# Kernel tuning notes

Measured on AMD Instinct MI355X. Metric: run time of the kernel, lower is better.

The kernel has to match this reference:

```python
import jax, jax.numpy as jnp
import numpy as np

# Static config (matches init_kwargs)
B = 1; Z = 64; H = 64; W = 64; C = 96
NH = 3; WS = 4; SS = 2
N = WS ** 3                      # tokens per 3D window = 64
NW = (Z // WS) * (H // WS) * (W // WS)   # num windows = 4096
SCALE = (C // NH) ** -0.5
EPS = 1e-5


def _rel_pos_index():
    # same construction as WindowAttention3D.__init__ (torch.meshgrid default 'ij')
    coords = np.stack(np.meshgrid(np.arange(WS), np.arange(WS), np.arange(WS), indexing='ij'))
    cf = coords.reshape(3, -1)                       # (3, N)
    rc = (cf[:, :, None] - cf[:, None, :]).transpose(1, 2, 0)  # (N, N, 3)
    rc[:, :, 0] += WS - 1; rc[:, :, 1] += WS - 1; rc[:, :, 2] += WS - 1
    rc[:, :, 0] *= (2 * WS - 1) ** 2
    rc[:, :, 1] *= (2 * WS - 1)
    return rc.sum(-1)                                # (N, N) int


def _attn_mask():
    # shifted-window mask, as in SwinTransformerBlock3D.__init__
    img = np.zeros((Z, H, W), dtype=np.float32)
    sl = (slice(0, -WS), slice(-WS, -SS), slice(-SS, None))
    cnt = 0
    for z in sl:
        for h in sl:
            for w in sl:
                img[z, h, w] = cnt
                cnt += 1
    mw = img.reshape(Z // WS, WS, H // WS, WS, W // WS, WS)
    mw = mw.transpose(0, 2, 4, 1, 3, 5).reshape(-1, N)        # (nW, N)
    am = mw[:, None, :] - mw[:, :, None]                      # (nW, N, N)
    return np.where(am != 0, np.float32(-100.0), np.float32(0.0))


REL_IDX = jnp.asarray(_rel_pos_index())        # (N, N) int32, closed-over constant
ATTN_MASK = jnp.asarray(_attn_mask())          # (nW, N, N) float32


def _layernorm(x, g, b):
    m = x.mean(-1, keepdims=True)
    v = ((x - m) ** 2).mean(-1, keepdims=True)
    return (x - m) * jax.lax.rsqrt(v + EPS) * g + b


def _window_partition(x):
    # (B, Z, H, W, C) -> (B*nW, N, C)
    x = x.reshape(B, Z // WS, WS, H // WS, WS, W // WS, WS, C)
    return x.transpose(0, 1, 3, 5, 2, 4, 6, 7).reshape(-1, N, C)


def _window_reverse(wins):
    # (B*nW, N, C) -> (B, Z, H, W, C)
    x = wins.reshape(B, Z // WS, H // WS, W // WS, WS, WS, WS, C)
    return x.transpose(0, 1, 4, 2, 5, 3, 6, 7).reshape(B, Z, H, W, C)


def setup_inputs() -> dict:
    key = jax.random.key(0)
    ks = jax.random.split(key, 8)
    d = {
        'x': jax.random.normal(ks[0], (B, Z * H * W, C), jnp.float32),
        'norm1_w': jnp.ones((C,), jnp.float32),
        'norm1_b': jnp.zeros((C,), jnp.float32),
        'qkv_w': jax.random.normal(ks[1], (3 * C, C), jnp.float32) * 0.02,
        'qkv_b': jnp.zeros((3 * C,), jnp.float32),
        'rel_bias': jax.random.normal(ks[2], ((2 * WS - 1) ** 3, NH), jnp.float32) * 0.02,
        'proj_w': jax.random.normal(ks[3], (C, C), jnp.float32) * 0.02,
        'proj_b': jnp.zeros((C,), jnp.float32),
        'norm2_w': jnp.ones((C,), jnp.float32),
        'norm2_b': jnp.zeros((C,), jnp.float32),
        'fc1_w': jax.random.normal(ks[4], (4 * C, C), jnp.float32) * 0.02,
        'fc1_b': jnp.zeros((4 * C,), jnp.float32),
        'fc2_w': jax.random.normal(ks[5], (C, 4 * C), jnp.float32) * 0.02,
        'fc2_b': jnp.zeros((C,), jnp.float32),
    }
    return d


def reference(x, norm1_w, norm1_b, qkv_w, qkv_b, rel_bias, proj_w, proj_b,
              norm2_w, norm2_b, fc1_w, fc1_b, fc2_w, fc2_b):
    shortcut = x
    h = _layernorm(x, norm1_w, norm1_b).reshape(B, Z, H, W, C)
    # cyclic shift (SW-MSA)
    h = jnp.roll(h, (-SS, -SS, -SS), axis=(1, 2, 3))
    xw = _window_partition(h)                                  # (B*nW, N, C)
    qkv = (xw @ qkv_w.T + qkv_b).reshape(-1, N, 3, NH, C // NH)
    qkv = qkv.transpose(2, 0, 3, 1, 4)                         # (3, B_, NH, N, hd)
    q, k, v = qkv[0] * SCALE, qkv[1], qkv[2]
    attn = jnp.einsum('bhnd,bhmd->bhnm', q, k)                 # (B_, NH, N, N)
    bias = rel_bias[REL_IDX.reshape(-1)].reshape(N, N, NH).transpose(2, 0, 1)
    attn = attn + bias[None]
    attn = attn.reshape(B, NW, NH, N, N) + ATTN_MASK[None, :, None]
    attn = jax.nn.softmax(attn.reshape(-1, NH, N, N), axis=-1)
    out = jnp.einsum('bhnm,bhmd->bhnd', attn, v)
    out = out.transpose(0, 2, 1, 3).reshape(-1, N, C)
    out = out @ proj_w.T + proj_b
    h = _window_reverse(out)
    h = jnp.roll(h, (SS, SS, SS), axis=(1, 2, 3)).reshape(B, Z * H * W, C)
    x = shortcut + h                                            # residual (drop_path=0)
    y = _layernorm(x, norm2_w, norm2_b)
    y = jax.nn.gelu(y @ fc1_w.T + fc1_b, approximate=False)
    y = y @ fc2_w.T + fc2_b
    return x + y
```

## Files before the change

kernel.cpp:

```cpp
#include <hip/hip_runtime.h>

typedef __attribute__((ext_vector_type(8))) short short8;
typedef __attribute__((ext_vector_type(4))) float f32x4;
typedef __attribute__((ext_vector_type(4))) unsigned short ush4;

static __device__ __forceinline__ unsigned short f2bf(float f) {
  return (unsigned short)((__builtin_bit_cast(unsigned int, f) + 0x8000u) >> 16);
}
static __device__ __forceinline__ unsigned cvtpk(float a, float b) {
  unsigned r;
  asm("v_cvt_pk_bf16_f32 %0, %1, %2" : "=v"(r) : "v"(a), "v"(b));
  return r;
}

constexpr float LOG2E = 1.4426950408889634f;
constexpr float QSCL = 0.17677669529663687f * LOG2E;
constexpr int XP = 104;
constexpr int KP = 104;
constexpr int VTP = 72;

static __device__ __forceinline__ int frag_src(int o, int K) {
  const int j = o & 7;
  const int lane = (o >> 3) & 63;
  const int f = o >> 9;
  const int nks = K >> 5;
  const int ks = f % nks;
  const int t = f / nks;
  const int row = t * 16 + (lane & 15);
  const int k = ks * 32 + (lane >> 4) * 8 + j;
  return row * K + k;
}

__global__ void prep_kernel(const float* __restrict__ qkvw, const float* __restrict__ projw,
                            const float* __restrict__ fc1w, const float* __restrict__ fc2w,
                            const float* __restrict__ relbias,
                            unsigned short* __restrict__ ws, float* __restrict__ tab) {
  int i = blockIdx.x * 256 + threadIdx.x;
  if (i < 27648) ws[i] = f2bf(qkvw[frag_src(i, 96)]);
  if (i < 9216)  ws[27648 + i] = f2bf(projw[frag_src(i, 96)]);
  if (i < 36864) {
    ws[36864 + i] = f2bf(fc1w[frag_src(i, 96)]);
    ws[73728 + i] = f2bf(fc2w[frag_src(i, 384)]);
  }
  if (i < 98304) {
    const int r = i & 3, kgi = (i >> 2) & 3, q = (i >> 4) & 63, nt = (i >> 10) & 3;
    const int vh = i >> 12;
    const int h = vh % 3, v = vh / 3;
    const int key = nt * 16 + kgi * 4 + r;
    const bool bz = v & 4, bh = v & 2, bw = v & 1;
    const int iz = q >> 4, ih = (q >> 2) & 3, iw = q & 3;
    const int jz = key >> 4, jh = (key >> 2) & 3, jw = key & 3;
    const int idx = (iz - jz + 3) * 49 + (ih - jh + 3) * 7 + (iw - jw + 3);
    const int ci = (bz ? (iz < 2 ? 9 : 18) : 0) + (bh ? (ih < 2 ? 3 : 6) : 0) +
                   (bw ? (iw < 2 ? 1 : 2) : 0);
    const int cj = (bz ? (jz < 2 ? 9 : 18) : 0) + (bh ? (jh < 2 ? 3 : 6) : 0) +
                   (bw ? (jw < 2 ? 1 : 2) : 0);
    tab[i] = (relbias[idx * 3 + h] + (ci != cj ? -100.f : 0.f)) * LOG2E;
  }
}

__global__ __launch_bounds__(256, 3) void fused_kernel(
    const float* __restrict__ x,
    const float* __restrict__ n1w, const float* __restrict__ n1b,
    const float* __restrict__ qkvb, const float* __restrict__ tab,
    const float* __restrict__ projb,
    const float* __restrict__ n2w, const float* __restrict__ n2b,
    const float* __restrict__ b1, const float* __restrict__ b2,
    const unsigned short* __restrict__ wq, const unsigned short* __restrict__ wp,
    const unsigned short* __restrict__ w1, const unsigned short* __restrict__ w2,
    float* __restrict__ out) {
  __shared__ unsigned short Xo[64 * XP];
  __shared__ unsigned short Kb[64 * KP];
  __shared__ unsigned short Vt[96 * VTP];

  const int tid = threadIdx.x;
  const int bid = blockIdx.x;
  const int wz = bid >> 8, wh = (bid >> 4) & 15, ww = bid & 15;
  const int wave = tid >> 6, lane = tid & 63;
  const int ln = lane & 15, kg = lane >> 4;

  {
    const int n = tid >> 2, part = tid & 3;
    const int lz = n >> 4, lh = (n >> 2) & 3, lw = n & 3;
    const int sz = (wz * 4 + lz + 2) & 63;
    const int sh = (wh * 4 + lh + 2) & 63;
    const int sw = (ww * 4 + lw + 2) & 63;
    const float* px = x + (size_t)((sz * 64 + sh) * 64 + sw) * 96 + part * 24;
    float4 v[6];
#pragma unroll
    for (int j = 0; j < 6; ++j) v[j] = ((const float4*)px)[j];
    float s = 0.f, sq = 0.f;
#pragma unroll
    for (int j = 0; j < 6; ++j) {
      s += v[j].x + v[j].y + v[j].z + v[j].w;
      sq += v[j].x * v[j].x + v[j].y * v[j].y + v[j].z * v[j].z + v[j].w * v[j].w;
    }
    s += __shfl_xor(s, 1);  s += __shfl_xor(s, 2);
    sq += __shfl_xor(sq, 1); sq += __shfl_xor(sq, 2);
    const float mean = s * (1.f / 96.f);
    const float var = sq * (1.f / 96.f) - mean * mean;
    const float rs = rsqrtf(var + 1e-5f);
    const float4* g4 = (const float4*)(n1w + part * 24);
    const float4* b4 = (const float4*)(n1b + part * 24);
#pragma unroll
    for (int j = 0; j < 6; ++j) {
      float4 g = g4[j], b = b4[j];
      uint2 o;
      o.x = cvtpk((v[j].x - mean) * rs * g.x + b.x, (v[j].y - mean) * rs * g.y + b.y);
      o.y = cvtpk((v[j].z - mean) * rs * g.z + b.z, (v[j].w - mean) * rs * g.w + b.w);
      *(uint2*)&Xo[n * XP + part * 24 + j * 4] = o;
    }
  }

  short8 qa[3];
  {
    short8 a[3];
#pragma unroll
    for (int ks = 0; ks < 3; ++ks)
      a[ks] = *(const short8*)&Xo[(wave * 16 + ln) * XP + ks * 32 + kg * 8];
#pragma unroll
    for (int half = 0; half < 2; ++half) {
      short8 wf[9];
#pragma unroll
      for (int f = 0; f < 9; ++f)
        wf[f] = *(const short8*)&wq[(size_t)(half * 9 + f) * 512 + lane * 8];
#pragma unroll
      for (int t = 0; t < 3; ++t) {
        const int nt = half * 3 + t;
        const int oc = nt * 16 + ln;
        f32x4 acc = {0.f, 0.f, 0.f, 0.f};
#pragma unroll
        for (int ks = 0; ks < 3; ++ks)
          acc = __builtin_amdgcn_mfma_f32_16x16x32_bf16(a[ks], wf[t * 3 + ks], acc, 0, 0, 0);
        const float bias = qkvb[oc];
#pragma unroll
        for (int r = 0; r < 4; ++r)
          Kb[(wave * 16 + kg * 4 + r) * KP + oc] = f2bf((acc[r] + bias) * QSCL);
      }
    }
#pragma unroll
    for (int h = 0; h < 3; ++h)
      qa[h] = *(const short8*)&Kb[(wave * 16 + ln) * KP + h * 32 + kg * 8];
#pragma unroll
    for (int half = 0; half < 2; ++half) {
      short8 wf[9];
#pragma unroll
      for (int f = 0; f < 9; ++f)
        wf[f] = *(const short8*)&wq[(size_t)(18 + half * 9 + f) * 512 + lane * 8];
#pragma unroll
      for (int t = 0; t < 3; ++t) {
        const int nt = half * 3 + t;
        const int oc = 96 + nt * 16 + ln;
        f32x4 acc = {0.f, 0.f, 0.f, 0.f};
#pragma unroll
        for (int ks = 0; ks < 3; ++ks)
          acc = __builtin_amdgcn_mfma_f32_16x16x32_bf16(a[ks], wf[t * 3 + ks], acc, 0, 0, 0);
        const float bias = qkvb[oc];
#pragma unroll
        for (int r = 0; r < 4; ++r)
          Kb[(wave * 16 + kg * 4 + r) * KP + nt * 16 + ln] = f2bf(acc[r] + bias);
      }
    }
#pragma unroll
    for (int half = 0; half < 2; ++half) {
      short8 wf[9];
#pragma unroll
      for (int f = 0; f < 9; ++f)
        wf[f] = *(const short8*)&wq[(size_t)(36 + half * 9 + f) * 512 + lane * 8];
#pragma unroll
      for (int t = 0; t < 3; ++t) {
        const int nt = half * 3 + t;
        const int oc = 192 + nt * 16 + ln;
        f32x4 acc = {0.f, 0.f, 0.f, 0.f};
#pragma unroll
        for (int ks = 0; ks < 3; ++ks)
          acc = __builtin_amdgcn_mfma_f32_16x16x32_bf16(a[ks], wf[t * 3 + ks], acc, 0, 0, 0);
        const float bias = qkvb[oc];
        uint2 u;
        u.x = cvtpk(acc[0] + bias, acc[1] + bias);
        u.y = cvtpk(acc[2] + bias, acc[3] + bias);
        *(uint2*)&Vt[(nt * 16 + ln) * VTP + wave * 16 + kg * 4] = u;
      }
    }
  }
  __syncthreads();

  const int vv = ((wz == 15) ? 4 : 0) | ((wh == 15) ? 2 : 0) | ((ww == 15) ? 1 : 0);
  const float* tb0 = tab + (size_t)(vv * 3) * 4096;
  const int rowbase = wave * 16 + kg * 4;
  const int lA = ((kg & 1) << 5) + ln;
  const int lB = lA + 16;
#pragma unroll
  for (int h = 0; h < 3; ++h) {
    const float* tb = tb0 + h * 4096;
    f32x4 trow[4];
#pragma unroll
    for (int nt = 0; nt < 4; ++nt)
      trow[nt] = *(const f32x4*)(tb + nt * 1024 + (wave * 16 + ln) * 16 + kg * 4);
    short8 kf[4];
#pragma unroll
    for (int nt = 0; nt < 4; ++nt)
      kf[nt] = *(const short8*)&Kb[(nt * 16 + ln) * KP + h * 32 + kg * 8];
    f32x4 e[4];
#pragma unroll
    for (int nt = 0; nt < 4; ++nt) {
      f32x4 z = {0.f, 0.f, 0.f, 0.f};
      f32x4 st = __builtin_amdgcn_mfma_f32_16x16x32_bf16(kf[nt], qa[h], z, 0, 0, 0);
#pragma unroll
      for (int r = 0; r < 4; ++r)
        e[nt][r] = __builtin_amdgcn_exp2f(st[r] + trow[nt][r]);
    }
    float hs = 0.f;
#pragma unroll
    for (int nt = 0; nt < 4; ++nt)
#pragma unroll
      for (int r = 0; r < 4; ++r) hs += e[nt][r];
    hs += __shfl_xor(hs, 16);
    hs += __shfl_xor(hs, 32);
    const float inv = __builtin_amdgcn_rcpf(hs);
    unsigned pp[4][2];
#pragma unroll
    for (int nt = 0; nt < 4; ++nt) {
      pp[nt][0] = cvtpk(e[nt][0] * inv, e[nt][1] * inv);
      pp[nt][1] = cvtpk(e[nt][2] * inv, e[nt][3] * inv);
    }
    short8 paf[2];
#pragma unroll
    for (int ks = 0; ks < 2; ++ks) {
      const unsigned a0 = __shfl((int)pp[2 * ks][0], lA);
      const unsigned a1 = __shfl((int)pp[2 * ks][1], lA);
      const unsigned a2 = __shfl((int)pp[2 * ks][0], lB);
      const unsigned a3 = __shfl((int)pp[2 * ks][1], lB);
      const unsigned b0 = __shfl((int)pp[2 * ks + 1][0], lA);
      const unsigned b1 = __shfl((int)pp[2 * ks + 1][1], lA);
      const unsigned b2 = __shfl((int)pp[2 * ks + 1][0], lB);
      const unsigned b3 = __shfl((int)pp[2 * ks + 1][1], lB);
      const bool hi = (kg >> 1) != 0;
      uint4 wv;
      wv.x = hi ? b0 : a0;
      wv.y = hi ? b1 : a1;
      wv.z = hi ? b2 : a2;
      wv.w = hi ? b3 : a3;
      paf[ks] = __builtin_bit_cast(short8, wv);
    }
#pragma unroll
    for (int dt = 0; dt < 2; ++dt) {
      f32x4 oacc = {0.f, 0.f, 0.f, 0.f};
#pragma unroll
      for (int ks = 0; ks < 2; ++ks) {
        short8 vb = *(const short8*)&Vt[(h * 32 + dt * 16 + ln) * VTP + ks * 32 + kg * 8];
        oacc = __builtin_amdgcn_mfma_f32_16x16x32_bf16(paf[ks], vb, oacc, 0, 0, 0);
      }
#pragma unroll
      for (int r = 0; r < 4; ++r)
        Xo[(rowbase + r) * XP + h * 32 + dt * 16 + ln] = f2bf(oacc[r]);
    }
  }

  float vout[6][4];
  int gtok[4];
  float mean_[4], rs_[4];
  {
#pragma unroll
    for (int r = 0; r < 4; ++r) {
      const int n = rowbase + r;
      const int lz = n >> 4, lh = (n >> 2) & 3, lw = n & 3;
      const int oz = (wz * 4 + lz + 2) & 63;
      const int oh = (wh * 4 + lh + 2) & 63;
      const int ow = (ww * 4 + lw + 2) & 63;
      gtok[r] = (oz * 64 + oh) * 64 + ow;
    }
    float xr[6][4];
#pragma unroll
    for (int nt = 0; nt < 6; ++nt)
#pragma unroll
      for (int r = 0; r < 4; ++r)
        xr[nt][r] = x[(size_t)gtok[r] * 96 + nt * 16 + ln];
    short8 oa[3];
#pragma unroll
    for (int ks = 0; ks < 3; ++ks)
      oa[ks] = *(const short8*)&Xo[(wave * 16 + ln) * XP + ks * 32 + kg * 8];
#pragma unroll
    for (int half = 0; half < 2; ++half) {
      short8 wf[9];
#pragma unroll
      for (int f = 0; f < 9; ++f)
        wf[f] = *(const short8*)&wp[(size_t)(half * 9 + f) * 512 + lane * 8];
#pragma unroll
      for (int t = 0; t < 3; ++t) {
        const int nt = half * 3 + t;
        const int col = nt * 16 + ln;
        f32x4 acc = {0.f, 0.f, 0.f, 0.f};
#pragma unroll
        for (int ks = 0; ks < 3; ++ks)
          acc = __builtin_amdgcn_mfma_f32_16x16x32_bf16(oa[ks], wf[t * 3 + ks], acc, 0, 0, 0);
        const float pbv = projb[col];
#pragma unroll
        for (int r = 0; r < 4; ++r)
          vout[nt][r] = xr[nt][r] + acc[r] + pbv;
      }
    }
#pragma unroll
    for (int r = 0; r < 4; ++r) {
      float s = 0.f, sq = 0.f;
#pragma unroll
      for (int nt = 0; nt < 6; ++nt) { s += vout[nt][r]; sq += vout[nt][r] * vout[nt][r]; }
      s += __shfl_xor(s, 1);  s += __shfl_xor(s, 2);
      s += __shfl_xor(s, 4);  s += __shfl_xor(s, 8);
      sq += __shfl_xor(sq, 1); sq += __shfl_xor(sq, 2);
      sq += __shfl_xor(sq, 4); sq += __shfl_xor(sq, 8);
      const float mean = s * (1.f / 96.f);
      const float var = sq * (1.f / 96.f) - mean * mean;
      mean_[r] = mean;
      rs_[r] = rsqrtf(var + 1e-5f);
    }
#pragma unroll
    for (int nt = 0; nt < 6; ++nt) {
      const int col = nt * 16 + ln;
      const float gw = n2w[col], gb = n2b[col];
#pragma unroll
      for (int r = 0; r < 4; ++r) {
        const float xl = (vout[nt][r] - mean_[r]) * rs_[r] * gw + gb;
        Xo[(rowbase + r) * XP + col] = f2bf(xl);
      }
    }
  }

  short8 a2[3];
#pragma unroll
  for (int ks = 0; ks < 3; ++ks)
    a2[ks] = *(const short8*)&Xo[(wave * 16 + ln) * XP + ks * 32 + kg * 8];

  __syncthreads();

  f32x4 facc[6];
#pragma unroll
  for (int nt = 0; nt < 6; ++nt) facc[nt] = (f32x4){0.f, 0.f, 0.f, 0.f};
#pragma unroll 1
  for (int c = 0; c < 4; ++c) {
#pragma unroll
    for (int half = 0; half < 2; ++half) {
      short8 wf1[9];
#pragma unroll
      for (int f = 0; f < 9; ++f)
        wf1[f] = *(const short8*)&w1[(size_t)(c * 18 + half * 9 + f) * 512 + lane * 8];
#pragma unroll
      for (int t = 0; t < 3; ++t) {
        const int nt2 = half * 3 + t;
        f32x4 acc = {0.f, 0.f, 0.f, 0.f};
#pragma unroll
        for (int ks = 0; ks < 3; ++ks)
          acc = __builtin_amdgcn_mfma_f32_16x16x32_bf16(a2[ks], wf1[t * 3 + ks], acc, 0, 0, 0);
        const float bb = b1[c * 96 + nt2 * 16 + ln];
#pragma unroll
        for (int r = 0; r < 4; ++r) {
          const float v = acc[r] + bb;
          const float t2 = v * v;
          float p = fmaf(0.004287f, t2, -0.05694f);
          p = fmaf(p, t2, 0.3952f);
          float phi = fmaf(p, v, 0.5f);
          phi = fminf(fmaxf(phi, 0.f), 1.f);
          Kb[(rowbase + r) * KP + nt2 * 16 + ln] = f2bf(v * phi);
        }
      }
    }
#pragma unroll
    for (int ks2 = 0; ks2 < 3; ++ks2) {
      short8 wf2[6];
#pragma unroll
      for (int nt = 0; nt < 6; ++nt)
        wf2[nt] = *(const short8*)&w2[(size_t)(nt * 12 + c * 3 + ks2) * 512 + lane * 8];
      short8 pa = *(const short8*)&Kb[(wave * 16 + ln) * KP + ks2 * 32 + kg * 8];
#pragma unroll
      for (int nt = 0; nt < 6; ++nt)
        facc[nt] = __builtin_amdgcn_mfma_f32_16x16x32_bf16(pa, wf2[nt], facc[nt], 0, 0, 0);
    }
  }
#pragma unroll
  for (int nt = 0; nt < 6; ++nt) {
    const int col = nt * 16 + ln;
    const float bb = b2[col];
#pragma unroll
    for (int r = 0; r < 4; ++r)
      out[(size_t)gtok[r] * 96 + col] = vout[nt][r] + facc[nt][r] + bb;
  }
}

extern "C" void kernel_launch(void* const* d_in, const int* in_sizes, int n_in,
                              void* d_out, int out_size, void* d_ws, size_t ws_size,
                              hipStream_t stream) {
  const float* x    = (const float*)d_in[0];
  const float* n1w  = (const float*)d_in[1];
  const float* n1b  = (const float*)d_in[2];
  const float* qkvw = (const float*)d_in[3];
  const float* qkvb = (const float*)d_in[4];
  const float* relb = (const float*)d_in[5];
  const float* pw   = (const float*)d_in[6];
  const float* pb   = (const float*)d_in[7];
  const float* n2w  = (const float*)d_in[8];
  const float* n2b  = (const float*)d_in[9];
  const float* w1   = (const float*)d_in[10];
  const float* b1   = (const float*)d_in[11];
  const float* w2   = (const float*)d_in[12];
  const float* b2   = (const float*)d_in[13];
  float* out = (float*)d_out;

  unsigned short* wsq = (unsigned short*)d_ws;
  unsigned short* wsp = wsq + 27648;
  unsigned short* ws1 = wsp + 9216;
  unsigned short* ws2 = ws1 + 36864;
  float* tab = (float*)(wsq + 110592);

  hipLaunchKernelGGL(prep_kernel, dim3(384), dim3(256), 0, stream,
                     qkvw, pw, w1, w2, relb, wsq, tab);
  hipLaunchKernelGGL(fused_kernel, dim3(4096), dim3(256), 0, stream,
                     x, n1w, n1b, qkvb, tab, pb, n2w, n2b, b1, b2,
                     wsq, wsp, ws1, ws2, out);
}
```

Baseline: 157.7 us.

## Cut register pressure to raise occupancy to four blocks per CU

Raises the launch bound from 3 to 4 blocks per CU. To fit that budget it shrinks the live register set. Weight fragments are now loaded in smaller groups, and the attention K and table loads move inside the per-tile loop. The post-attention residual is no longer held in a 24-float array: it is written to the output buffer, reread for LayerNorm2, and read back again for the final residual add. This trades extra global memory traffic and smaller load batches, which hide latency less well, for more resident waves.

```diff
diff --git a/kernel.cpp b/kernel.cpp
--- a/kernel.cpp
+++ b/kernel.cpp
@@ -2,7 +2,6 @@
 
 typedef __attribute__((ext_vector_type(8))) short short8;
 typedef __attribute__((ext_vector_type(4))) float f32x4;
-typedef __attribute__((ext_vector_type(4))) unsigned short ush4;
 
 static __device__ __forceinline__ unsigned short f2bf(float f) {
   return (unsigned short)((__builtin_bit_cast(unsigned int, f) + 0x8000u) >> 16);
@@ -59,7 +58,7 @@
   }
 }
 
-__global__ __launch_bounds__(256, 3) void fused_kernel(
+__global__ __launch_bounds__(256, 4) void fused_kernel(
     const float* __restrict__ x,
     const float* __restrict__ n1w, const float* __restrict__ n1b,
     const float* __restrict__ qkvb, const float* __restrict__ tab,
@@ -119,14 +118,14 @@
     for (int ks = 0; ks < 3; ++ks)
       a[ks] = *(const short8*)&Xo[(wave * 16 + ln) * XP + ks * 32 + kg * 8];
 #pragma unroll
-    for (int half = 0; half < 2; ++half) {
-      short8 wf[9];
-#pragma unroll
-      for (int f = 0; f < 9; ++f)
-        wf[f] = *(const short8*)&wq[(size_t)(half * 9 + f) * 512 + lane * 8];
-#pragma unroll
-      for (int t = 0; t < 3; ++t) {
-        const int nt = half * 3 + t;
+    for (int g = 0; g < 3; ++g) {
+      short8 wf[6];
+#pragma unroll
+      for (int f = 0; f < 6; ++f)
+        wf[f] = *(const short8*)&wq[(size_t)(g * 6 + f) * 512 + lane * 8];
+#pragma unroll
+      for (int t = 0; t < 2; ++t) {
+        const int nt = g * 2 + t;
         const int oc = nt * 16 + ln;
         f32x4 acc = {0.f, 0.f, 0.f, 0.f};
 #pragma unroll
@@ -142,14 +141,14 @@
     for (int h = 0; h < 3; ++h)
       qa[h] = *(const short8*)&Kb[(wave * 16 + ln) * KP + h * 32 + kg * 8];
 #pragma unroll
-    for (int half = 0; half < 2; ++half) {
-      short8 wf[9];
-#pragma unroll
-      for (int f = 0; f < 9; ++f)
-        wf[f] = *(const short8*)&wq[(size_t)(18 + half * 9 + f) * 512 + lane * 8];
-#pragma unroll
-      for (int t = 0; t < 3; ++t) {
-        const int nt = half * 3 + t;
+    for (int g = 0; g < 3; ++g) {
+      short8 wf[6];
+#pragma unroll
+      for (int f = 0; f < 6; ++f)
+        wf[f] = *(const short8*)&wq[(size_t)(18 + g * 6 + f) * 512 + lane * 8];
+#pragma unroll
+      for (int t = 0; t < 2; ++t) {
+        const int nt = g * 2 + t;
         const int oc = 96 + nt * 16 + ln;
         f32x4 acc = {0.f, 0.f, 0.f, 0.f};
 #pragma unroll
@@ -162,14 +161,14 @@
       }
     }
 #pragma unroll
-    for (int half = 0; half < 2; ++half) {
-      short8 wf[9];
-#pragma unroll
-      for (int f = 0; f < 9; ++f)
-        wf[f] = *(const short8*)&wq[(size_t)(36 + half * 9 + f) * 512 + lane * 8];
-#pragma unroll
-      for (int t = 0; t < 3; ++t) {
-        const int nt = half * 3 + t;
+    for (int g = 0; g < 3; ++g) {
+      short8 wf[6];
+#pragma unroll
+      for (int f = 0; f < 6; ++f)
+        wf[f] = *(const short8*)&wq[(size_t)(36 + g * 6 + f) * 512 + lane * 8];
+#pragma unroll
+      for (int t = 0; t < 2; ++t) {
+        const int nt = g * 2 + t;
         const int oc = 192 + nt * 16 + ln;
         f32x4 acc = {0.f, 0.f, 0.f, 0.f};
 #pragma unroll
@@ -193,22 +192,16 @@
 #pragma unroll
   for (int h = 0; h < 3; ++h) {
     const float* tb = tb0 + h * 4096;
-    f32x4 trow[4];
-#pragma unroll
-    for (int nt = 0; nt < 4; ++nt)
-      trow[nt] = *(const f32x4*)(tb + nt * 1024 + (wave * 16 + ln) * 16 + kg * 4);
-    short8 kf[4];
-#pragma unroll
-    for (int nt = 0; nt < 4; ++nt)
-      kf[nt] = *(const short8*)&Kb[(nt * 16 + ln) * KP + h * 32 + kg * 8];
     f32x4 e[4];
 #pragma unroll
     for (int nt = 0; nt < 4; ++nt) {
+      short8 kf = *(const short8*)&Kb[(nt * 16 + ln) * KP + h * 32 + kg * 8];
+      f32x4 trow = *(const f32x4*)(tb + nt * 1024 + (wave * 16 + ln) * 16 + kg * 4);
       f32x4 z = {0.f, 0.f, 0.f, 0.f};
-      f32x4 st = __builtin_amdgcn_mfma_f32_16x16x32_bf16(kf[nt], qa[h], z, 0, 0, 0);
+      f32x4 st = __builtin_amdgcn_mfma_f32_16x16x32_bf16(kf, qa[h], z, 0, 0, 0);
 #pragma unroll
       for (int r = 0; r < 4; ++r)
-        e[nt][r] = __builtin_amdgcn_exp2f(st[r] + trow[nt][r]);
+        e[nt][r] = __builtin_amdgcn_exp2f(st[r] + trow[r]);
     }
     float hs = 0.f;
 #pragma unroll
@@ -257,7 +250,6 @@
     }
   }
 
-  float vout[6][4];
   int gtok[4];
   float mean_[4], rs_[4];
   {
@@ -270,25 +262,20 @@
       const int ow = (ww * 4 + lw + 2) & 63;
       gtok[r] = (oz * 64 + oh) * 64 + ow;
     }
-    float xr[6][4];
-#pragma unroll
-    for (int nt = 0; nt < 6; ++nt)
-#pragma unroll
-      for (int r = 0; r < 4; ++r)
-        xr[nt][r] = x[(size_t)gtok[r] * 96 + nt * 16 + ln];
     short8 oa[3];
 #pragma unroll
     for (int ks = 0; ks < 3; ++ks)
       oa[ks] = *(const short8*)&Xo[(wave * 16 + ln) * XP + ks * 32 + kg * 8];
-#pragma unroll
-    for (int half = 0; half < 2; ++half) {
-      short8 wf[9];
-#pragma unroll
-      for (int f = 0; f < 9; ++f)
-        wf[f] = *(const short8*)&wp[(size_t)(half * 9 + f) * 512 + lane * 8];
-#pragma unroll
-      for (int t = 0; t < 3; ++t) {
-        const int nt = half * 3 + t;
+    float s_[4] = {0.f, 0.f, 0.f, 0.f}, sq_[4] = {0.f, 0.f, 0.f, 0.f};
+#pragma unroll
+    for (int g = 0; g < 3; ++g) {
+      short8 wf[6];
+#pragma unroll
+      for (int f = 0; f < 6; ++f)
+        wf[f] = *(const short8*)&wp[(size_t)(g * 6 + f) * 512 + lane * 8];
+#pragma unroll
+      for (int t = 0; t < 2; ++t) {
+        const int nt = g * 2 + t;
         const int col = nt * 16 + ln;
         f32x4 acc = {0.f, 0.f, 0.f, 0.f};
 #pragma unroll
@@ -296,15 +283,17 @@
           acc = __builtin_amdgcn_mfma_f32_16x16x32_bf16(oa[ks], wf[t * 3 + ks], acc, 0, 0, 0);
         const float pbv = projb[col];
 #pragma unroll
-        for (int r = 0; r < 4; ++r)
-          vout[nt][r] = xr[nt][r] + acc[r] + pbv;
+        for (int r = 0; r < 4; ++r) {
+          const float v = x[(size_t)gtok[r] * 96 + col] + acc[r] + pbv;
+          s_[r] += v;
+          sq_[r] += v * v;
+          out[(size_t)gtok[r] * 96 + col] = v;
+        }
       }
     }
 #pragma unroll
     for (int r = 0; r < 4; ++r) {
-      float s = 0.f, sq = 0.f;
-#pragma unroll
-      for (int nt = 0; nt < 6; ++nt) { s += vout[nt][r]; sq += vout[nt][r] * vout[nt][r]; }
+      float s = s_[r], sq = sq_[r];
       s += __shfl_xor(s, 1);  s += __shfl_xor(s, 2);
       s += __shfl_xor(s, 4);  s += __shfl_xor(s, 8);
       sq += __shfl_xor(sq, 1); sq += __shfl_xor(sq, 2);
@@ -314,15 +303,16 @@
       mean_[r] = mean;
       rs_[r] = rsqrtf(var + 1e-5f);
     }
-#pragma unroll
-    for (int nt = 0; nt < 6; ++nt) {
-      const int col = nt * 16 + ln;
-      const float gw = n2w[col], gb = n2b[col];
-#pragma unroll
-      for (int r = 0; r < 4; ++r) {
-        const float xl = (vout[nt][r] - mean_[r]) * rs_[r] * gw + gb;
-        Xo[(rowbase + r) * XP + col] = f2bf(xl);
-      }
+  }
+#pragma unroll
+  for (int nt = 0; nt < 6; ++nt) {
+    const int col = nt * 16 + ln;
+    const float gw = n2w[col], gb = n2b[col];
+#pragma unroll
+    for (int r = 0; r < 4; ++r) {
+      const float v = out[(size_t)gtok[r] * 96 + col];
+      const float xl = (v - mean_[r]) * rs_[r] * gw + gb;
+      Xo[(rowbase + r) * XP + col] = f2bf(xl);
     }
   }
 
@@ -339,41 +329,41 @@
 #pragma unroll 1
   for (int c = 0; c < 4; ++c) {
 #pragma unroll
-    for (int half = 0; half < 2; ++half) {
-      short8 wf1[9];
-#pragma unroll
-      for (int f = 0; f < 9; ++f)
-        wf1[f] = *(const short8*)&w1[(size_t)(c * 18 + half * 9 + f) * 512 + lane * 8];
-#pragma unroll
-      for (int t = 0; t < 3; ++t) {
-        const int nt2 = half * 3 + t;
-        f32x4 acc = {0.f, 0.f, 0.f, 0.f};
-#pragma unroll
-        for (int ks = 0; ks < 3; ++ks)
-          acc = __builtin_amdgcn_mfma_f32_16x16x32_bf16(a2[ks], wf1[t * 3 + ks], acc, 0, 0, 0);
-        const float bb = b1[c * 96 + nt2 * 16 + ln];
-#pragma unroll
-        for (int r = 0; r < 4; ++r) {
-          const float v = acc[r] + bb;
-          const float t2 = v * v;
-          float p = fmaf(0.004287f, t2, -0.05694f);
-          p = fmaf(p, t2, 0.3952f);
-          float phi = fmaf(p, v, 0.5f);
-          phi = fminf(fmaxf(phi, 0.f), 1.f);
-          Kb[(rowbase + r) * KP + nt2 * 16 + ln] = f2bf(v * phi);
-        }
+    for (int nt2 = 0; nt2 < 6; ++nt2) {
+      short8 wf1[3];
+#pragma unroll
+      for (int ks = 0; ks < 3; ++ks)
+        wf1[ks] = *(const short8*)&w1[(size_t)(c * 18 + nt2 * 3 + ks) * 512 + lane * 8];
+      f32x4 acc = {0.f, 0.f, 0.f, 0.f};
+#pragma unroll
+      for (int ks = 0; ks < 3; ++ks)
+        acc = __builtin_amdgcn_mfma_f32_16x16x32_bf16(a2[ks], wf1[ks], acc, 0, 0, 0);
+      const float bb = b1[c * 96 + nt2 * 16 + ln];
+#pragma unroll
+      for (int r = 0; r < 4; ++r) {
+        const float v = acc[r] + bb;
+        const float t2 = v * v;
+        float p = fmaf(0.004287f, t2, -0.05694f);
+        p = fmaf(p, t2, 0.3952f);
+        float phi = fmaf(p, v, 0.5f);
+        phi = fminf(fmaxf(phi, 0.f), 1.f);
+        Kb[(rowbase + r) * KP + nt2 * 16 + ln] = f2bf(v * phi);
       }
     }
 #pragma unroll
     for (int ks2 = 0; ks2 < 3; ++ks2) {
-      short8 wf2[6];
-#pragma unroll
-      for (int nt = 0; nt < 6; ++nt)
-        wf2[nt] = *(const short8*)&w2[(size_t)(nt * 12 + c * 3 + ks2) * 512 + lane * 8];
       short8 pa = *(const short8*)&Kb[(wave * 16 + ln) * KP + ks2 * 32 + kg * 8];
 #pragma unroll
-      for (int nt = 0; nt < 6; ++nt)
-        facc[nt] = __builtin_amdgcn_mfma_f32_16x16x32_bf16(pa, wf2[nt], facc[nt], 0, 0, 0);
+      for (int g2 = 0; g2 < 2; ++g2) {
+        short8 wf2[3];
+#pragma unroll
+        for (int t = 0; t < 3; ++t)
+          wf2[t] = *(const short8*)&w2[(size_t)((g2 * 3 + t) * 12 + c * 3 + ks2) * 512 + lane * 8];
+#pragma unroll
+        for (int t = 0; t < 3; ++t)
+          facc[g2 * 3 + t] =
+              __builtin_amdgcn_mfma_f32_16x16x32_bf16(pa, wf2[t], facc[g2 * 3 + t], 0, 0, 0);
+      }
     }
   }
 #pragma unroll
@@ -381,8 +371,10 @@
     const int col = nt * 16 + ln;
     const float bb = b2[col];
 #pragma unroll
-    for (int r = 0; r < 4; ++r)
-      out[(size_t)gtok[r] * 96 + col] = vout[nt][r] + facc[nt][r] + bb;
+    for (int r = 0; r < 4; ++r) {
+      const size_t idx = (size_t)gtok[r] * 96 + col;
+      out[idx] = out[idx] + facc[nt][r] + bb;
+    }
   }
 }
 
```

Result: slower. 193.3 us (+22.5%).
